# Performance work log

Hardware: AMD Instinct MI355X
Metric: run time of the kernel (lower is better)

The kernel has to match this reference:

```python
import math
import jax, jax.numpy as jnp
import numpy as np

QUERY_DIM = 768
FEAT_DIM = 1024
HID_DIM = 768
OUT_DIM = 768
B, L, S, T = 32, 256, 64, 64


def _linear_params(key, fan_in, fan_out):
    kw, kb = jax.random.split(key)
    scale = 1.0 / math.sqrt(fan_in)
    W = jax.random.uniform(kw, (fan_in, fan_out), jnp.float32, -scale, scale)
    b = jax.random.uniform(kb, (fan_out,), jnp.float32, -scale, scale)
    return W, b


def setup_inputs() -> dict:
    key = jax.random.key(0)
    ks = jax.random.split(key, 7)
    query = jax.random.normal(ks[0], (B, L, QUERY_DIM), jnp.float32)
    src = jax.random.normal(ks[1], (B, S, FEAT_DIM), jnp.float32)
    trg = jax.random.normal(ks[2], (B, T, FEAT_DIM), jnp.float32)
    Wq, b_q = _linear_params(ks[3], QUERY_DIM, HID_DIM)
    Ws, b_s = _linear_params(ks[4], FEAT_DIM, HID_DIM)
    Wt, b_t = _linear_params(ks[5], FEAT_DIM, HID_DIM)
    Wo, b_o = _linear_params(ks[6], HID_DIM + QUERY_DIM, OUT_DIM)
    return {"query": query, "src": src, "trg": trg,
            "Wq": Wq, "b_q": b_q, "Ws": Ws, "b_s": b_s,
            "Wt": Wt, "b_t": b_t, "Wo": Wo, "b_o": b_o}


def reference(query, src, trg, Wq, b_q, Ws, b_s, Wt, b_t, Wo, b_o):
    # Projections (LinearAct with identity activation).
    q = query @ Wq + b_q          # (b, l, h)
    s_key = src @ Ws + b_s        # (b, s, h)
    t_key = trg @ Wt + b_t        # (b, t, h)
    # rel_key[b, t, s, h] = tanh(s_key[b, s, h] + t_key[b, t, h])
    rel_key = jnp.tanh(s_key[:, None, :, :] + t_key[:, :, None, :])  # (b, t, s, h)
    # Scores over combined (t, s) positions.
    weight = jnp.einsum('blk,btsk->blts', q, rel_key) / math.sqrt(HID_DIM)  # (b, l, t, s)
    b_, l_, t_, s_ = weight.shape
    weight = jax.nn.softmax(weight.reshape(b_, l_, t_ * s_), axis=-1).reshape(b_, l_, t_, s_)
    # Context: weighted sum of rel_key over (t, s).
    rel_ctx = jnp.einsum('blts,btsk->blk', weight, rel_key)  # (b, l, h)
    x = jnp.concatenate([query, rel_ctx], axis=-1)           # (b, l, h + q)
    return jax.nn.relu(x @ Wo + b_o)                          # (b, l, out)
```

## Files before the change

### kernel.cpp

```cpp
#include <hip/hip_runtime.h>
#include <math.h>


typedef __attribute__((ext_vector_type(8))) short bf16x8;
typedef __attribute__((ext_vector_type(4))) float f32x4;

__device__ __forceinline__ unsigned short f2bf(float f) {
    union { float f; unsigned u; } x; x.f = f;
    unsigned u = x.u;
    return (unsigned short)((u + 0x7fffu + ((u >> 16) & 1u)) >> 16);
}
__device__ __forceinline__ float bf2f(unsigned short h) {
    union { unsigned u; float f; } x; x.u = (unsigned)h << 16;
    return x.f;
}
__device__ __forceinline__ float tanh_fast(float x) {
    float e = __expf(2.0f * x);
    return 1.0f - 2.0f * __builtin_amdgcn_rcpf(1.0f + e);
}
__device__ __forceinline__ void async_copy16(void* lds, const void* g) {
    __builtin_amdgcn_global_load_lds(
        (const __attribute__((address_space(1))) unsigned int*)g,
        (__attribute__((address_space(3))) unsigned int*)lds,
        16, 0, 0);
}

template<bool OUT_BF16, bool RELU>
__global__ __launch_bounds__(256, 2) void gemm_bt_kernel(
    const unsigned short* __restrict__ A, const unsigned short* __restrict__ BT,
    void* __restrict__ Cout, const float* __restrict__ bias,
    int M, int N, int K, int lda, int ldb, int ldc,
    long long sA, long long sB, long long sC)
{
    __shared__ unsigned short As[128 * 32];
    __shared__ unsigned short Bs[128 * 32];
    const int z = blockIdx.z;
    A  += (long long)z * sA;
    BT += (long long)z * sB;
    const int m0 = blockIdx.x * 128, n0 = blockIdx.y * 128;
    const int tid = threadIdx.x;
    const int lane = tid & 63, wid = tid >> 6;
    const int wr = wid >> 1, wc = wid & 1;
    const int r = lane & 15, g = lane >> 4;

    f32x4 acc[4][4] = {};

    for (int k0 = 0; k0 < K; k0 += 32) {
        __syncthreads();
        #pragma unroll
        for (int j = 0; j < 2; ++j) {
            int c = j * 256 + tid;
            int row = c >> 2, kc = (c & 3) * 8;
            async_copy16(&As[c * 8], A  + (size_t)(m0 + row) * lda + k0 + kc);
            async_copy16(&Bs[c * 8], BT + (size_t)(n0 + row) * ldb + k0 + kc);
        }
        asm volatile("s_waitcnt vmcnt(0)" ::: "memory");
        __syncthreads();

        bf16x8 af[4], bfr[4];
        #pragma unroll
        for (int m = 0; m < 4; ++m)
            af[m] = *(const bf16x8*)&As[(wr * 64 + m * 16 + r) * 32 + g * 8];
        #pragma unroll
        for (int n = 0; n < 4; ++n)
            bfr[n] = *(const bf16x8*)&Bs[(wc * 64 + n * 16 + r) * 32 + g * 8];
        #pragma unroll
        for (int m = 0; m < 4; ++m)
            #pragma unroll
            for (int n = 0; n < 4; ++n)
                acc[m][n] = __builtin_amdgcn_mfma_f32_16x16x32_bf16(
                    af[m], bfr[n], acc[m][n], 0, 0, 0);
    }

    float* Cf = (float*)Cout;
    unsigned short* Cb = (unsigned short*)Cout;
    const long long cbase = (long long)z * sC;
    #pragma unroll
    for (int n = 0; n < 4; ++n) {
        int col = n0 + wc * 64 + n * 16 + r;
        float bv = bias ? bias[col] : 0.0f;
        #pragma unroll
        for (int m = 0; m < 4; ++m) {
            int row0 = m0 + wr * 64 + m * 16 + g * 4;
            #pragma unroll
            for (int i = 0; i < 4; ++i) {
                float v = acc[m][n][i] + bv;
                if (RELU) v = fmaxf(v, 0.0f);
                size_t off = (size_t)cbase + (size_t)(row0 + i) * ldc + col;
                if (OUT_BF16) Cb[off] = f2bf(v);
                else          Cf[off] = v;
            }
        }
    }
}

__global__ __launch_bounds__(256, 2) void scores_kernel(
    const unsigned short* __restrict__ qh,
    const float* __restrict__ s_key,
    const float* __restrict__ t_key,
    unsigned short* __restrict__ scores)
{
    __shared__ unsigned short As[128 * 32];
    __shared__ unsigned short Bs[128 * 40];
    __shared__ float Sk[64 * 36];
    __shared__ float Tk[2 * 32];

    const int b = blockIdx.z;
    const unsigned short* A = qh + (size_t)b * 256 * 768;
    const float* skp = s_key + (size_t)b * 64 * 768;
    const float* tkp = t_key + (size_t)b * 64 * 768;
    const int m0 = blockIdx.x * 128, n0 = blockIdx.y * 128;
    const int t0 = n0 >> 6;
    const int tid = threadIdx.x;
    const int lane = tid & 63, wid = tid >> 6;
    const int wr = wid >> 1, wc = wid & 1;
    const int r = lane & 15, g = lane >> 4;

    f32x4 acc[4][4] = {};

    for (int k0 = 0; k0 < 768; k0 += 32) {
        __syncthreads();
        if (tid < 64) Tk[tid] = tkp[(size_t)(t0 + (tid >> 5)) * 768 + k0 + (tid & 31)];
        #pragma unroll
        for (int j = 0; j < 2; ++j) {
            int c = j * 256 + tid;
            int row = c >> 2, kc = (c & 3) * 8;
            async_copy16(&As[c * 8], A + (size_t)(m0 + row) * 768 + k0 + kc);
        }
        {
            int s = tid >> 2, c4 = (tid & 3) * 8;
            float4 v0 = *(const float4*)&skp[(size_t)s * 768 + k0 + c4];
            float4 v1 = *(const float4*)&skp[(size_t)s * 768 + k0 + c4 + 4];
            *(float4*)&Sk[s * 36 + c4]     = v0;
            *(float4*)&Sk[s * 36 + c4 + 4] = v1;
        }
        asm volatile("s_waitcnt vmcnt(0)" ::: "memory");
        __syncthreads();

        #pragma unroll
        for (int j = 0; j < 2; ++j) {
            int c = j * 256 + tid;
            int n = c >> 2, kc = (c & 3) * 8;
            const float* sv = &Sk[(n & 63) * 36 + kc];
            const float* tv = &Tk[(n >> 6) * 32 + kc];
            bf16x8 o;
            #pragma unroll
            for (int e = 0; e < 8; ++e)
                o[e] = (short)f2bf(tanh_fast(sv[e] + tv[e]));
            *(bf16x8*)&Bs[n * 40 + kc] = o;
        }
        __syncthreads();

        bf16x8 af[4], bfr[4];
        #pragma unroll
        for (int m = 0; m < 4; ++m)
            af[m] = *(const bf16x8*)&As[(wr * 64 + m * 16 + r) * 32 + g * 8];
        #pragma unroll
        for (int n = 0; n < 4; ++n)
            bfr[n] = *(const bf16x8*)&Bs[(wc * 64 + n * 16 + r) * 40 + g * 8];
        #pragma unroll
        for (int m = 0; m < 4; ++m)
            #pragma unroll
            for (int n = 0; n < 4; ++n)
                acc[m][n] = __builtin_amdgcn_mfma_f32_16x16x32_bf16(
                    af[m], bfr[n], acc[m][n], 0, 0, 0);
    }

    unsigned short* C = scores + (size_t)b * 256 * 4096;
    #pragma unroll
    for (int n = 0; n < 4; ++n) {
        int col = n0 + wc * 64 + n * 16 + r;
        #pragma unroll
        for (int m = 0; m < 4; ++m) {
            int row0 = m0 + wr * 64 + m * 16 + g * 4;
            #pragma unroll
            for (int i = 0; i < 4; ++i)
                C[(size_t)(row0 + i) * 4096 + col] = f2bf(acc[m][n][i]);
        }
    }
}

__global__ __launch_bounds__(256, 3) void ctx_kernel(
    const unsigned short* __restrict__ w,
    const float* __restrict__ s_key,
    const float* __restrict__ t_key,
    unsigned short* __restrict__ xcat)
{
    __shared__ unsigned short As[128 * 32];
    __shared__ unsigned short Bs[64 * 40];

    const int b = blockIdx.z;
    const unsigned short* A = w + (size_t)b * 256 * 4096;
    const float* skp = s_key + (size_t)b * 64 * 768;
    const float* tkp = t_key + (size_t)b * 64 * 768;
    const int m0 = blockIdx.x * 128, n0 = blockIdx.y * 64;
    const int tid = threadIdx.x;
    const int lane = tid & 63, wid = tid >> 6;
    const int wr = wid >> 1, wc = wid & 1;
    const int r = lane & 15, g = lane >> 4;
    const int sl = tid & 31, hg = tid >> 5;

    f32x4 acc[4][2] = {};

    for (int k0 = 0; k0 < 4096; k0 += 32) {
        const int t = k0 >> 6, s = (k0 & 63) + sl;
        __syncthreads();
        #pragma unroll
        for (int j = 0; j < 2; ++j) {
            int c = j * 256 + tid;
            int row = c >> 2, kc = (c & 3) * 8;
            async_copy16(&As[c * 8], A + (size_t)(m0 + row) * 4096 + k0 + kc);
        }
        {
            const float* sv = &skp[(size_t)s * 768 + n0 + hg * 8];
            const float* tv = &tkp[(size_t)t * 768 + n0 + hg * 8];
            float4 sa = *(const float4*)sv, sb = *(const float4*)(sv + 4);
            float4 ta = *(const float4*)tv, tb = *(const float4*)(tv + 4);
            Bs[(hg * 8 + 0) * 40 + sl] = f2bf(tanh_fast(sa.x + ta.x));
            Bs[(hg * 8 + 1) * 40 + sl] = f2bf(tanh_fast(sa.y + ta.y));
            Bs[(hg * 8 + 2) * 40 + sl] = f2bf(tanh_fast(sa.z + ta.z));
            Bs[(hg * 8 + 3) * 40 + sl] = f2bf(tanh_fast(sa.w + ta.w));
            Bs[(hg * 8 + 4) * 40 + sl] = f2bf(tanh_fast(sb.x + tb.x));
            Bs[(hg * 8 + 5) * 40 + sl] = f2bf(tanh_fast(sb.y + tb.y));
            Bs[(hg * 8 + 6) * 40 + sl] = f2bf(tanh_fast(sb.z + tb.z));
            Bs[(hg * 8 + 7) * 40 + sl] = f2bf(tanh_fast(sb.w + tb.w));
        }
        asm volatile("s_waitcnt vmcnt(0)" ::: "memory");
        __syncthreads();

        bf16x8 af[4], bfr[2];
        #pragma unroll
        for (int m = 0; m < 4; ++m)
            af[m] = *(const bf16x8*)&As[(wr * 64 + m * 16 + r) * 32 + g * 8];
        #pragma unroll
        for (int n = 0; n < 2; ++n)
            bfr[n] = *(const bf16x8*)&Bs[(wc * 32 + n * 16 + r) * 40 + g * 8];
        #pragma unroll
        for (int m = 0; m < 4; ++m)
            #pragma unroll
            for (int n = 0; n < 2; ++n)
                acc[m][n] = __builtin_amdgcn_mfma_f32_16x16x32_bf16(
                    af[m], bfr[n], acc[m][n], 0, 0, 0);
    }

    unsigned short* C = xcat + (size_t)b * 256 * 1536 + 768;
    #pragma unroll
    for (int n = 0; n < 2; ++n) {
        int col = n0 + wc * 32 + n * 16 + r;
        #pragma unroll
        for (int m = 0; m < 4; ++m) {
            int row0 = m0 + wr * 64 + m * 16 + g * 4;
            #pragma unroll
            for (int i = 0; i < 4; ++i)
                C[(size_t)(row0 + i) * 1536 + col] = f2bf(acc[m][n][i]);
        }
    }
}

__global__ void cvt_bf16_kernel(const float* __restrict__ in,
                                unsigned short* __restrict__ out, int n4) {
    int i = blockIdx.x * 256 + threadIdx.x;
    if (i >= n4) return;
    float4 v = ((const float4*)in)[i];
    ushort4 o;
    o.x = f2bf(v.x); o.y = f2bf(v.y); o.z = f2bf(v.z); o.w = f2bf(v.w);
    ((ushort4*)out)[i] = o;
}

__global__ void cvt_query_kernel(const float* __restrict__ in,
                                 unsigned short* __restrict__ xcat) {
    int i = blockIdx.x * 256 + threadIdx.x;
    if (i >= 8192 * 192) return;
    int row = i / 192, c4 = (i % 192) * 4;
    float4 v = ((const float4*)in)[i];
    ushort4 o;
    o.x = f2bf(v.x); o.y = f2bf(v.y); o.z = f2bf(v.z); o.w = f2bf(v.w);
    *(ushort4*)&xcat[(size_t)row * 1536 + c4] = o;
}

__global__ void transpose_w_kernel(const float* __restrict__ in,
                                   unsigned short* __restrict__ out,
                                   int R, int C) {
    __shared__ float tile[64][65];
    const int r0 = blockIdx.y * 64, c0 = blockIdx.x * 64;
    const int tx = threadIdx.x & 63, ty = threadIdx.x >> 6;
    for (int i = ty; i < 64; i += 4)
        tile[i][tx] = in[(size_t)(r0 + i) * C + c0 + tx];
    __syncthreads();
    for (int i = ty; i < 64; i += 4)
        out[(size_t)(c0 + i) * R + r0 + tx] = f2bf(tile[tx][i]);
}

__global__ __launch_bounds__(256) void softmax_kernel(unsigned short* __restrict__ scores) {
    unsigned short* p = scores + (size_t)blockIdx.x * 4096;
    const int tid = threadIdx.x, lane = tid & 63, wid = tid >> 6;
    __shared__ float red[4];

    float v[16];
    {
        const bf16x8* p8 = (const bf16x8*)p;
        bf16x8 a = p8[tid * 2], c = p8[tid * 2 + 1];
        #pragma unroll
        for (int e = 0; e < 8; ++e) {
            v[e]     = bf2f((unsigned short)a[e]);
            v[8 + e] = bf2f((unsigned short)c[e]);
        }
    }
    float mx = v[0];
    #pragma unroll
    for (int e = 1; e < 16; ++e) mx = fmaxf(mx, v[e]);
    #pragma unroll
    for (int o = 32; o; o >>= 1) mx = fmaxf(mx, __shfl_xor(mx, o));
    if (lane == 0) red[wid] = mx;
    __syncthreads();
    mx = fmaxf(fmaxf(red[0], red[1]), fmaxf(red[2], red[3]));
    __syncthreads();

    const float scale = 0.03608439182435161f;
    float sum = 0.0f;
    #pragma unroll
    for (int e = 0; e < 16; ++e) {
        v[e] = __expf((v[e] - mx) * scale);
        sum += v[e];
    }
    #pragma unroll
    for (int o = 32; o; o >>= 1) sum += __shfl_xor(sum, o);
    if (lane == 0) red[wid] = sum;
    __syncthreads();
    sum = red[0] + red[1] + red[2] + red[3];
    const float inv = 1.0f / sum;

    bf16x8* p8 = (bf16x8*)p;
    #pragma unroll
    for (int j = 0; j < 2; ++j) {
        bf16x8 o;
        #pragma unroll
        for (int e = 0; e < 8; ++e)
            o[e] = (short)f2bf(v[j * 8 + e] * inv);
        p8[tid * 2 + j] = o;
    }
}

extern "C" void kernel_launch(void* const* d_in, const int* in_sizes, int n_in,
                              void* d_out, int out_size, void* d_ws, size_t ws_size,
                              hipStream_t stream) {
    const float* query = (const float*)d_in[0];
    const float* src   = (const float*)d_in[1];
    const float* trg   = (const float*)d_in[2];
    const float* Wq    = (const float*)d_in[3];
    const float* b_q   = (const float*)d_in[4];
    const float* Ws    = (const float*)d_in[5];
    const float* b_s   = (const float*)d_in[6];
    const float* Wt    = (const float*)d_in[7];
    const float* b_t   = (const float*)d_in[8];
    const float* Wo    = (const float*)d_in[9];
    const float* b_o   = (const float*)d_in[10];

    char* ws = (char*)d_ws;
    size_t off = 0;
    auto alloc = [&](size_t bytes) {
        void* p = ws + off;
        off += (bytes + 255) & ~(size_t)255;
        return p;
    };
    unsigned short* xcat   = (unsigned short*)alloc((size_t)8192 * 1536 * 2);
    unsigned short* srcbf  = (unsigned short*)alloc((size_t)2048 * 1024 * 2);
    unsigned short* trgbf  = (unsigned short*)alloc((size_t)2048 * 1024 * 2);
    unsigned short* WqT    = (unsigned short*)alloc((size_t)768 * 768 * 2);
    unsigned short* WsT    = (unsigned short*)alloc((size_t)768 * 1024 * 2);
    unsigned short* WtT    = (unsigned short*)alloc((size_t)768 * 1024 * 2);
    unsigned short* WoT    = (unsigned short*)alloc((size_t)768 * 1536 * 2);
    unsigned short* qh     = (unsigned short*)alloc((size_t)8192 * 768 * 2);
    float*          s_key  = (float*)alloc((size_t)2048 * 768 * 4);
    float*          t_key  = (float*)alloc((size_t)2048 * 768 * 4);
    unsigned short* scores = (unsigned short*)alloc((size_t)32 * 256 * 4096 * 2);

    cvt_query_kernel<<<6144, 256, 0, stream>>>(query, xcat);
    cvt_bf16_kernel<<<2048, 256, 0, stream>>>(src, srcbf, 524288);
    cvt_bf16_kernel<<<2048, 256, 0, stream>>>(trg, trgbf, 524288);

    transpose_w_kernel<<<dim3(12, 12), 256, 0, stream>>>(Wq, WqT, 768, 768);
    transpose_w_kernel<<<dim3(12, 16), 256, 0, stream>>>(Ws, WsT, 1024, 768);
    transpose_w_kernel<<<dim3(12, 16), 256, 0, stream>>>(Wt, WtT, 1024, 768);
    transpose_w_kernel<<<dim3(12, 24), 256, 0, stream>>>(Wo, WoT, 1536, 768);

    gemm_bt_kernel<true, false><<<dim3(64, 6, 1), 256, 0, stream>>>(
        xcat, WqT, qh, b_q, 8192, 768, 768, 1536, 768, 768, 0, 0, 0);
    gemm_bt_kernel<false, false><<<dim3(16, 6, 1), 256, 0, stream>>>(
        srcbf, WsT, s_key, b_s, 2048, 768, 1024, 1024, 1024, 768, 0, 0, 0);
    gemm_bt_kernel<false, false><<<dim3(16, 6, 1), 256, 0, stream>>>(
        trgbf, WtT, t_key, b_t, 2048, 768, 1024, 1024, 1024, 768, 0, 0, 0);

    scores_kernel<<<dim3(2, 32, 32), 256, 0, stream>>>(qh, s_key, t_key, scores);

    softmax_kernel<<<8192, 256, 0, stream>>>(scores);

    ctx_kernel<<<dim3(2, 12, 32), 256, 0, stream>>>(scores, s_key, t_key, xcat);

    gemm_bt_kernel<false, true><<<dim3(64, 6, 1), 256, 0, stream>>>(
        xcat, WoT, d_out, b_o, 8192, 768, 1536, 1536, 1536, 768, 0, 0, 0);
}
```

Measured before the change: 524.1 us.

## Double-buffer weight tiles with XOR swizzle and process full t-row per iteration in ctx_kernel

The context GEMM kernel now works on one full t row (K=64) per iteration instead of K=32. The A (softmax weight) tile is prefetched asynchronously into a second LDS buffer while the current one is consumed. The A tile uses an XOR-swizzled LDS layout to avoid bank conflicts when reading MFMA fragments, and the tanh-generated B tile covers both s halves per step. This halves the barrier count and hides global load latency, at the cost of more LDS per block (about 42 KB vs 13 KB), which may lower occupancy below the declared 3 blocks per CU.

After: 462.4 us. -11.8%, faster.

```diff
diff --git a/kernel.cpp b/kernel.cpp
--- a/kernel.cpp
+++ b/kernel.cpp
@@ -186,8 +186,8 @@
     const float* __restrict__ t_key,
     unsigned short* __restrict__ xcat)
 {
-    __shared__ unsigned short As[128 * 32];
-    __shared__ unsigned short Bs[64 * 40];
+    __shared__ unsigned short As[2][128 * 64];
+    __shared__ unsigned short Bs[2][64 * 40];
 
     const int b = blockIdx.z;
     const unsigned short* A = w + (size_t)b * 256 * 4096;
@@ -200,47 +200,81 @@
     const int r = lane & 15, g = lane >> 4;
     const int sl = tid & 31, hg = tid >> 5;
 
+    auto stage = [&](int d, int t) {
+        #pragma unroll
+        for (int j = 0; j < 4; ++j) {
+            int c = j * 256 + tid;
+            int row = c >> 3, pcol = c & 7;
+            int gcol = pcol ^ (row & 7);
+            async_copy16(&As[d][c * 8],
+                         A + (size_t)(m0 + row) * 4096 + t * 64 + gcol * 8);
+        }
+    };
+
     f32x4 acc[4][2] = {};
 
-    for (int k0 = 0; k0 < 4096; k0 += 32) {
-        const int t = k0 >> 6, s = (k0 & 63) + sl;
-        __syncthreads();
-        #pragma unroll
-        for (int j = 0; j < 2; ++j) {
-            int c = j * 256 + tid;
-            int row = c >> 2, kc = (c & 3) * 8;
-            async_copy16(&As[c * 8], A + (size_t)(m0 + row) * 4096 + k0 + kc);
-        }
+    stage(0, 0);
+    asm volatile("s_waitcnt vmcnt(0)" ::: "memory");
+    __syncthreads();
+
+    for (int t = 0; t < 64; ++t) {
+        const int cur = t & 1;
+
+        const float* tvp = &tkp[(size_t)t * 768 + n0 + hg * 8];
+        float4 ta = *(const float4*)tvp, tb = *(const float4*)(tvp + 4);
+        const float* sv0 = &skp[(size_t)sl * 768 + n0 + hg * 8];
+        const float* sv1 = &skp[(size_t)(32 + sl) * 768 + n0 + hg * 8];
+        float4 sa0 = *(const float4*)sv0, sb0 = *(const float4*)(sv0 + 4);
+        float4 sa1 = *(const float4*)sv1, sb1 = *(const float4*)(sv1 + 4);
+
+        if (t < 63) stage(cur ^ 1, t + 1);
+
         {
-            const float* sv = &skp[(size_t)s * 768 + n0 + hg * 8];
-            const float* tv = &tkp[(size_t)t * 768 + n0 + hg * 8];
-            float4 sa = *(const float4*)sv, sb = *(const float4*)(sv + 4);
-            float4 ta = *(const float4*)tv, tb = *(const float4*)(tv + 4);
-            Bs[(hg * 8 + 0) * 40 + sl] = f2bf(tanh_fast(sa.x + ta.x));
-            Bs[(hg * 8 + 1) * 40 + sl] = f2bf(tanh_fast(sa.y + ta.y));
-            Bs[(hg * 8 + 2) * 40 + sl] = f2bf(tanh_fast(sa.z + ta.z));
-            Bs[(hg * 8 + 3) * 40 + sl] = f2bf(tanh_fast(sa.w + ta.w));
-            Bs[(hg * 8 + 4) * 40 + sl] = f2bf(tanh_fast(sb.x + tb.x));
-            Bs[(hg * 8 + 5) * 40 + sl] = f2bf(tanh_fast(sb.y + tb.y));
-            Bs[(hg * 8 + 6) * 40 + sl] = f2bf(tanh_fast(sb.z + tb.z));
-            Bs[(hg * 8 + 7) * 40 + sl] = f2bf(tanh_fast(sb.w + tb.w));
-        }
-        asm volatile("s_waitcnt vmcnt(0)" ::: "memory");
-        __syncthreads();
-
-        bf16x8 af[4], bfr[2];
-        #pragma unroll
-        for (int m = 0; m < 4; ++m)
-            af[m] = *(const bf16x8*)&As[(wr * 64 + m * 16 + r) * 32 + g * 8];
-        #pragma unroll
-        for (int n = 0; n < 2; ++n)
-            bfr[n] = *(const bf16x8*)&Bs[(wc * 32 + n * 16 + r) * 40 + g * 8];
-        #pragma unroll
-        for (int m = 0; m < 4; ++m)
+            int hb = hg * 8;
+            Bs[0][(hb + 0) * 40 + sl] = f2bf(tanh_fast(sa0.x + ta.x));
+            Bs[0][(hb + 1) * 40 + sl] = f2bf(tanh_fast(sa0.y + ta.y));
+            Bs[0][(hb + 2) * 40 + sl] = f2bf(tanh_fast(sa0.z + ta.z));
+            Bs[0][(hb + 3) * 40 + sl] = f2bf(tanh_fast(sa0.w + ta.w));
+            Bs[0][(hb + 4) * 40 + sl] = f2bf(tanh_fast(sb0.x + tb.x));
+            Bs[0][(hb + 5) * 40 + sl] = f2bf(tanh_fast(sb0.y + tb.y));
+            Bs[0][(hb + 6) * 40 + sl] = f2bf(tanh_fast(sb0.z + tb.z));
+            Bs[0][(hb + 7) * 40 + sl] = f2bf(tanh_fast(sb0.w + tb.w));
+            Bs[1][(hb + 0) * 40 + sl] = f2bf(tanh_fast(sa1.x + ta.x));
+            Bs[1][(hb + 1) * 40 + sl] = f2bf(tanh_fast(sa1.y + ta.y));
+            Bs[1][(hb + 2) * 40 + sl] = f2bf(tanh_fast(sa1.z + ta.z));
+            Bs[1][(hb + 3) * 40 + sl] = f2bf(tanh_fast(sa1.w + ta.w));
+            Bs[1][(hb + 4) * 40 + sl] = f2bf(tanh_fast(sb1.x + tb.x));
+            Bs[1][(hb + 5) * 40 + sl] = f2bf(tanh_fast(sb1.y + tb.y));
+            Bs[1][(hb + 6) * 40 + sl] = f2bf(tanh_fast(sb1.z + tb.z));
+            Bs[1][(hb + 7) * 40 + sl] = f2bf(tanh_fast(sb1.w + tb.w));
+        }
+
+        asm volatile("s_waitcnt lgkmcnt(0)" ::: "memory");
+        __builtin_amdgcn_sched_barrier(0);
+        __builtin_amdgcn_s_barrier();
+        __builtin_amdgcn_sched_barrier(0);
+
+        #pragma unroll
+        for (int kk = 0; kk < 2; ++kk) {
+            bf16x8 af[4], bfr[2];
+            #pragma unroll
+            for (int m = 0; m < 4; ++m) {
+                int rowr = wr * 64 + m * 16 + r;
+                int phys = (kk * 4 + g) ^ (rowr & 7);
+                af[m] = *(const bf16x8*)&As[cur][rowr * 64 + phys * 8];
+            }
             #pragma unroll
             for (int n = 0; n < 2; ++n)
-                acc[m][n] = __builtin_amdgcn_mfma_f32_16x16x32_bf16(
-                    af[m], bfr[n], acc[m][n], 0, 0, 0);
+                bfr[n] = *(const bf16x8*)&Bs[kk][(wc * 32 + n * 16 + r) * 40 + g * 8];
+            #pragma unroll
+            for (int m = 0; m < 4; ++m)
+                #pragma unroll
+                for (int n = 0; n < 2; ++n)
+                    acc[m][n] = __builtin_amdgcn_mfma_f32_16x16x32_bf16(
+                        af[m], bfr[n], acc[m][n], 0, 0, 0);
+        }
+
+        __syncthreads();
     }
 
     unsigned short* C = xcat + (size_t)b * 256 * 1536 + 768;
```
